# Performance work log

Measured on AMD Instinct MI355X. Metric: run time of the kernel, lower is better.

The kernel has to match this reference:

```python
import jax, jax.numpy as jnp
import numpy as np

BS, T, HS, WS = 2, 4, 32, 32
HW = HS * WS
D, NH, NL, NP = 256, 8, 4, 4
HD = D // NH
DFFN = 1024


def layer_norm(x, g, b, eps=1e-5):
    mu = jnp.mean(x, axis=-1, keepdims=True)
    var = jnp.mean((x - mu) ** 2, axis=-1, keepdims=True)
    return (x - mu) * jax.lax.rsqrt(var + eps) * g + b


def bilinear_gather(val, loc, Hl, Wl):
    # val: (bs, nh, Hl*Wl, hd); loc: (bs, Lq, nh, P, 2) in [0,1], last dim (x, y)
    # matches F.grid_sample(align_corners=False, padding_mode='zeros') on grid=2*loc-1
    x = loc[..., 0] * Wl - 0.5
    y = loc[..., 1] * Hl - 0.5
    x0 = jnp.floor(x)
    y0 = jnp.floor(y)
    lx = x - x0
    ly = y - y0
    bs, Lq, nh, P = x.shape
    out = jnp.zeros((bs, nh, Lq * P, val.shape[-1]), val.dtype)
    for dy in (0, 1):
        for dx in (0, 1):
            xi = x0 + dx
            yi = y0 + dy
            w = (lx if dx else 1.0 - lx) * (ly if dy else 1.0 - ly)
            valid = (xi >= 0) & (xi < Wl) & (yi >= 0) & (yi < Hl)
            w = jnp.where(valid, w, 0.0)
            xi_c = jnp.clip(xi, 0, Wl - 1).astype(jnp.int32)
            yi_c = jnp.clip(yi, 0, Hl - 1).astype(jnp.int32)
            idx = (yi_c * Wl + xi_c).transpose(0, 2, 1, 3).reshape(bs, nh, Lq * P)
            g = jnp.take_along_axis(val, idx[..., None], axis=2)
            wt = w.transpose(0, 2, 1, 3).reshape(bs, nh, Lq * P)
            out = out + wt[..., None] * g
    return out.reshape(bs, nh, Lq, P, val.shape[-1])


def setup_inputs() -> dict:
    key = jax.random.key(0)
    ks = jax.random.split(key, 12)
    s = 0.02
    return {
        "src": jax.random.normal(ks[0], (BS, T, HW, D), jnp.float32),
        "pos": jax.random.normal(ks[1], (BS, T, HW, D), jnp.float32),
        "reference_points": jax.random.uniform(ks[2], (BS, T * HW, NL, 2), jnp.float32),
        "value_proj_w": jax.random.normal(ks[3], (D, D), jnp.float32) * s,
        "value_proj_b": jnp.zeros((D,), jnp.float32),
        "sampling_offsets_w": jax.random.normal(ks[4], (D, NH * NL * NP * 2), jnp.float32) * s,
        "sampling_offsets_b": jax.random.normal(ks[5], (NH * NL * NP * 2,), jnp.float32) * s,
        "attn_weights_w": jax.random.normal(ks[6], (D, NH * NL * NP), jnp.float32) * s,
        "attn_weights_b": jnp.zeros((NH * NL * NP,), jnp.float32),
        "output_proj_w": jax.random.normal(ks[7], (D, D), jnp.float32) * s,
        "output_proj_b": jnp.zeros((D,), jnp.float32),
        "norm1_g": jnp.ones((D,), jnp.float32),
        "norm1_b": jnp.zeros((D,), jnp.float32),
        "linear1_w": jax.random.normal(ks[8], (D, DFFN), jnp.float32) * s,
        "linear1_b": jnp.zeros((DFFN,), jnp.float32),
        "linear2_w": jax.random.normal(ks[9], (DFFN, D), jnp.float32) * s,
        "linear2_b": jnp.zeros((D,), jnp.float32),
        "norm2_g": jnp.ones((D,), jnp.float32),
        "norm2_b": jnp.zeros((D,), jnp.float32),
        "spatial_shapes": np.array([[HS, WS]] * NL, np.int32),
        "level_start_index": np.arange(NL, dtype=np.int32) * HW,
    }


def reference(src, pos, reference_points, value_proj_w, value_proj_b,
              sampling_offsets_w, sampling_offsets_b, attn_weights_w, attn_weights_b,
              output_proj_w, output_proj_b, norm1_g, norm1_b,
              linear1_w, linear1_b, linear2_w, linear2_b, norm2_g, norm2_b,
              spatial_shapes, level_start_index):
    bs, t, hw, d = src.shape
    Lq = t * hw
    x = src.reshape(bs, Lq, d)
    q = x  # module never adds pos in forward (with_pos_embed unused)
    value = (x @ value_proj_w + value_proj_b).reshape(bs, Lq, NH, HD)
    offsets = (q @ sampling_offsets_w + sampling_offsets_b).reshape(bs, Lq, NH, NL, NP, 2)
    aw = jax.nn.softmax((q @ attn_weights_w + attn_weights_b).reshape(bs, Lq, NH, NL * NP), axis=-1)
    aw = aw.reshape(bs, Lq, NH, NL, NP)
    ss = np.asarray(spatial_shapes)
    lsi = np.asarray(level_start_index)
    offset_normalizer = jnp.asarray(ss[:, ::-1].copy(), src.dtype)  # (L, 2) = (W, H)
    sampling_locations = reference_points[:, :, None, :, None, :] + offsets / offset_normalizer[None, None, None, :, None, :]
    attn_out = jnp.zeros((bs, NH, Lq, HD), src.dtype)
    for l in range(NL):
        Hl, Wl = int(ss[l, 0]), int(ss[l, 1])
        start = int(lsi[l])
        v_l = value[:, start:start + Hl * Wl].transpose(0, 2, 1, 3)  # (bs, nh, HlWl, hd)
        samp = bilinear_gather(v_l, sampling_locations[:, :, :, l], Hl, Wl)  # (bs, nh, Lq, P, hd)
        w_l = aw[:, :, :, l].transpose(0, 2, 1, 3)  # (bs, nh, Lq, P)
        attn_out = attn_out + jnp.sum(samp * w_l[..., None], axis=3)
    attn_out = attn_out.transpose(0, 2, 1, 3).reshape(bs, Lq, d) @ output_proj_w + output_proj_b
    x = layer_norm(x + attn_out, norm1_g, norm1_b)
    ffn = jax.nn.relu(x @ linear1_w + linear1_b) @ linear2_w + linear2_b
    x = layer_norm(x + ffn, norm2_g, norm2_b)
    return x.reshape(bs, t, hw, d), sampling_locations
```

## Files before the change

### kernel.cpp

```cpp
#include <hip/hip_runtime.h>
#include <math.h>

#define ROWS   8192
#define LQ     4096
#define NHEAD  8
#define NLVL   4
#define NPTS   4
#define HDIM   32

typedef __attribute__((ext_vector_type(8))) short v8s;
typedef __attribute__((ext_vector_type(4))) float v4f;

__device__ __forceinline__ unsigned short f2bf(float x) {
    unsigned int u = __float_as_uint(x);
    u += 0x7fffu + ((u >> 16) & 1u);
    return (unsigned short)(u >> 16);
}
__device__ __forceinline__ float bf2f(unsigned short x) {
    return __uint_as_float(((unsigned int)x) << 16);
}

__device__ __forceinline__ void glds16(const void* g, void* l) {
    __builtin_amdgcn_global_load_lds(
        (const __attribute__((address_space(1))) unsigned int*)g,
        (__attribute__((address_space(3))) unsigned int*)l, 16, 0, 0);
}

__device__ __forceinline__ void trans_tile(const float* __restrict__ in,
                                           unsigned short* __restrict__ out,
                                           int K, int N, int ldout, int n_off,
                                           int bx, int by, int tid)
{
    __shared__ float t[32][33];
    int tx = tid & 31, ty = tid >> 5;
    int k0 = by << 5, n0 = bx << 5;
    #pragma unroll
    for (int i = 0; i < 4; i++)
        t[ty + i * 8][tx] = in[(size_t)(k0 + ty + i * 8) * N + n0 + tx];
    __syncthreads();
    #pragma unroll
    for (int i = 0; i < 4; i++)
        out[(size_t)(n_off + n0 + ty + i * 8) * ldout + k0 + tx] = f2bf(t[tx][ty + i * 8]);
}

__global__ __launch_bounds__(256) void prep_k(
    const float* __restrict__ src, unsigned short* __restrict__ src_bf,
    const float* __restrict__ vw, const float* __restrict__ ofw,
    const float* __restrict__ aww, const float* __restrict__ pw,
    const float* __restrict__ w1, const float* __restrict__ w2,
    unsigned short* __restrict__ Btcat, unsigned short* __restrict__ pwT,
    unsigned short* __restrict__ w1T, unsigned short* __restrict__ w2T,
    const float* __restrict__ vb, const float* __restrict__ ofb,
    const float* __restrict__ awb, float* __restrict__ biascat)
{
    int bid = blockIdx.x, tid = threadIdx.x;
    if (bid < 2048) {
        int i = bid * 256 + tid;
        float4 v = ((const float4*)src)[i];
        ushort4 o;
        o.x = f2bf(v.x); o.y = f2bf(v.y); o.z = f2bf(v.z); o.w = f2bf(v.w);
        ((ushort4*)src_bf)[i] = o;
    } else if (bid < 2112) {
        int t = bid - 2048; trans_tile(vw, Btcat, 256, 256, 256, 0, t & 7, t >> 3, tid);
    } else if (bid < 2176) {
        int t = bid - 2112; trans_tile(ofw, Btcat, 256, 256, 256, 256, t & 7, t >> 3, tid);
    } else if (bid < 2208) {
        int t = bid - 2176; trans_tile(aww, Btcat, 256, 128, 256, 512, t & 3, t >> 2, tid);
    } else if (bid < 2272) {
        int t = bid - 2208; trans_tile(pw, pwT, 256, 256, 256, 0, t & 7, t >> 3, tid);
    } else if (bid < 2528) {
        int t = bid - 2272; trans_tile(w1, w1T, 256, 1024, 256, 0, t & 31, t >> 5, tid);
    } else if (bid < 2784) {
        int t = bid - 2528; trans_tile(w2, w2T, 1024, 256, 1024, 0, t & 7, t >> 3, tid);
    } else {
        biascat[tid] = vb[tid];
        biascat[tid + 256] = ofb[tid];
        if (tid < 128) biascat[tid + 512] = awb[tid];
    }
}

template<bool PROJ, bool OUTBF, bool RELU, bool RES>
__global__ __launch_bounds__(256) void mfma_gemm_k(
    const unsigned short* __restrict__ A,
    const unsigned short* __restrict__ Bt,
    const float* __restrict__ bias,
    const float* __restrict__ res,
    void* __restrict__ Cout,
    unsigned short* __restrict__ vbf,
    int M, int N, int K)
{
    __shared__ __align__(16) unsigned short As[4096];
    __shared__ __align__(16) unsigned short Bs[2048];
    const int tid = threadIdx.x;
    const int row0 = blockIdx.y << 7, col0 = blockIdx.x << 6;
    const int wid = tid >> 6, lane = tid & 63;
    const int wm = wid & 1, wn = wid >> 1;
    const int lr = lane & 15, kq = lane >> 4;

    v4f acc[4][2];
    #pragma unroll
    for (int i = 0; i < 4; i++)
        #pragma unroll
        for (int j = 0; j < 2; j++) acc[i][j] = (v4f){0.f, 0.f, 0.f, 0.f};

    for (int k0 = 0; k0 < K; k0 += 32) {
        __syncthreads();
        #pragma unroll
        for (int i = 0; i < 2; i++) {
            int c = wid * 128 + i * 64 + lane;
            int row = c >> 2;
            int kk = ((c & 3) + (row >> 2)) & 3;
            glds16(A + (size_t)(row0 + row) * K + k0 + kk * 8,
                   &As[(wid * 128 + i * 64) * 8]);
        }
        {
            int c = wid * 64 + lane;
            int row = c >> 2;
            int kk = ((c & 3) + (row >> 2)) & 3;
            glds16(Bt + (size_t)(col0 + row) * K + k0 + kk * 8,
                   &Bs[wid * 512]);
        }
        __syncthreads();
        v8s bf[2];
        #pragma unroll
        for (int nt = 0; nt < 2; nt++) {
            int row = wn * 32 + nt * 16 + lr;
            int s = (kq - (row >> 2)) & 3;
            bf[nt] = *(const v8s*)(&Bs[(row * 4 + s) * 8]);
        }
        #pragma unroll
        for (int mt = 0; mt < 4; mt++) {
            int row = wm * 64 + mt * 16 + lr;
            int s = (kq - (row >> 2)) & 3;
            v8s af = *(const v8s*)(&As[(row * 4 + s) * 8]);
            #pragma unroll
            for (int nt = 0; nt < 2; nt++)
                acc[mt][nt] = __builtin_amdgcn_mfma_f32_16x16x32_bf16(af, bf[nt], acc[mt][nt], 0, 0, 0);
        }
    }

    const int rq = lane >> 4;
    #pragma unroll
    for (int mt = 0; mt < 4; mt++) {
        #pragma unroll
        for (int nt = 0; nt < 2; nt++) {
            int col = col0 + wn * 32 + nt * 16 + lr;
            float bv = bias[col];
            #pragma unroll
            for (int i = 0; i < 4; i++) {
                int row = row0 + wm * 64 + mt * 16 + rq * 4 + i;
                float v = acc[mt][nt][i] + bv;
                if (RELU) v = fmaxf(v, 0.f);
                if (RES)  v += res[(size_t)row * N + col];
                if (PROJ) {
                    if (col0 < 256) {
                        int b = row >> 12, rb = row & 4095;
                        int l = rb >> 10, pix = rb & 1023;
                        int h = col >> 5, d = col & 31;
                        size_t idx = ((size_t)(((b << 2) + l) * 8 + h) << 15) + (pix << 5) + d;
                        vbf[idx] = f2bf(v);
                    } else {
                        ((float*)Cout)[(size_t)row * 384 + col - 256] = v;
                    }
                } else if (OUTBF) {
                    ((unsigned short*)Cout)[(size_t)row * N + col] = f2bf(v);
                } else {
                    ((float*)Cout)[(size_t)row * N + col] = v;
                }
            }
        }
    }
}

__global__ __launch_bounds__(256) void fused_gather_k(
    const float* __restrict__ po,
    const unsigned short* __restrict__ vbf,
    const float* __restrict__ refp,
    float* __restrict__ out_loc,
    unsigned short* __restrict__ attn_bf)
{
    int tid = threadIdx.x;
    int u = tid >> 5, l = (tid >> 3) & 3, d4 = tid & 7;
    int gid = blockIdx.x * 8 + u;
    int h = gid & 7, r = gid >> 3;
    int b = r >> 12;
    const float* prow = po + (size_t)r * 384;

    float2 rp = *(const float2*)(refp + (size_t)r * 8 + l * 2);

    float off[8];
    *(float4*)(off)     = *(const float4*)(prow + h * 32 + l * 8);
    *(float4*)(off + 4) = *(const float4*)(prow + h * 32 + l * 8 + 4);
    float locv[8];
    #pragma unroll
    for (int k = 0; k < 8; k++)
        locv[k] = ((k & 1) ? rp.y : rp.x) + off[k] * (1.f / 32.f);
    out_loc[(size_t)r * 256 + h * 32 + l * 8 + d4] = locv[d4];

    float w4[4];
    *(float4*)(w4) = *(const float4*)(prow + 256 + h * 16 + l * 4);
    float m = fmaxf(fmaxf(w4[0], w4[1]), fmaxf(w4[2], w4[3]));
    m = fmaxf(m, __shfl_xor(m, 8));
    m = fmaxf(m, __shfl_xor(m, 16));
    float s = 0.f;
    #pragma unroll
    for (int p = 0; p < 4; p++) { w4[p] = __expf(w4[p] - m); s += w4[p]; }
    s += __shfl_xor(s, 8);
    s += __shfl_xor(s, 16);
    float inv = 1.f / s;

    const unsigned short* vbase =
        vbf + (((size_t)(((b << 2) + l) * 8 + h)) << 15) + d4 * 4;
    ushort4 uv[16];
    float cw[16];
    #pragma unroll
    for (int p = 0; p < 4; p++) {
        float xf = locv[p * 2] * 32.f - 0.5f, yf = locv[p * 2 + 1] * 32.f - 0.5f;
        float x0f = floorf(xf), y0f = floorf(yf);
        float fx = xf - x0f, fy = yf - y0f;
        int x0 = (int)x0f, y0 = (int)y0f;
        float wgt = w4[p] * inv;
        #pragma unroll
        for (int dy = 0; dy < 2; dy++) {
            #pragma unroll
            for (int dx = 0; dx < 2; dx++) {
                int idx = p * 4 + dy * 2 + dx;
                int xi = x0 + dx, yi = y0 + dy;
                float wt = (dx ? fx : 1.f - fx) * (dy ? fy : 1.f - fy);
                bool valid = (xi >= 0) & (xi < 32) & (yi >= 0) & (yi < 32);
                int xc = min(max(xi, 0), 31), yc = min(max(yi, 0), 31);
                cw[idx] = valid ? (wgt * wt) : 0.f;
                uv[idx] = *(const ushort4*)(vbase + (size_t)((yc << 5) + xc) * 32);
            }
        }
    }
    float4 acc = {0.f, 0.f, 0.f, 0.f};
    #pragma unroll
    for (int idx = 0; idx < 16; idx++) {
        float c = cw[idx];
        acc.x += c * bf2f(uv[idx].x); acc.y += c * bf2f(uv[idx].y);
        acc.z += c * bf2f(uv[idx].z); acc.w += c * bf2f(uv[idx].w);
    }
    acc.x += __shfl_xor(acc.x, 8);  acc.y += __shfl_xor(acc.y, 8);
    acc.z += __shfl_xor(acc.z, 8);  acc.w += __shfl_xor(acc.w, 8);
    acc.x += __shfl_xor(acc.x, 16); acc.y += __shfl_xor(acc.y, 16);
    acc.z += __shfl_xor(acc.z, 16); acc.w += __shfl_xor(acc.w, 16);
    if (l == 0) {
        ushort4 o;
        o.x = f2bf(acc.x); o.y = f2bf(acc.y); o.z = f2bf(acc.z); o.w = f2bf(acc.w);
        *(ushort4*)(attn_bf + (size_t)r * 256 + h * 32 + d4 * 4) = o;
    }
}

template<bool WRITE_BF>
__global__ __launch_bounds__(256) void layernorm_k(
    float* __restrict__ x, const float* __restrict__ g, const float* __restrict__ b,
    unsigned short* __restrict__ xbf)
{
    int lane = threadIdx.x & 63;
    int wv = threadIdx.x >> 6;
    int row = blockIdx.x * 4 + wv;
    int c = lane << 2;
    float4 v = *(const float4*)(x + (size_t)row * 256 + c);
    float s = v.x + v.y + v.z + v.w;
    #pragma unroll
    for (int o = 1; o < 64; o <<= 1) s += __shfl_xor(s, o);
    float mu = s * (1.f / 256.f);
    float d0 = v.x - mu, d1 = v.y - mu, d2 = v.z - mu, d3 = v.w - mu;
    float vs = d0 * d0 + d1 * d1 + d2 * d2 + d3 * d3;
    #pragma unroll
    for (int o = 1; o < 64; o <<= 1) vs += __shfl_xor(vs, o);
    float rstd = rsqrtf(vs * (1.f / 256.f) + 1e-5f);
    float4 gg = *(const float4*)(g + c);
    float4 bb = *(const float4*)(b + c);
    float4 o4;
    o4.x = d0 * rstd * gg.x + bb.x;
    o4.y = d1 * rstd * gg.y + bb.y;
    o4.z = d2 * rstd * gg.z + bb.z;
    o4.w = d3 * rstd * gg.w + bb.w;
    *(float4*)(x + (size_t)row * 256 + c) = o4;
    if (WRITE_BF) {
        ushort4 ob;
        ob.x = f2bf(o4.x); ob.y = f2bf(o4.y); ob.z = f2bf(o4.z); ob.w = f2bf(o4.w);
        *(ushort4*)(xbf + (size_t)row * 256 + c) = ob;
    }
}

extern "C" void kernel_launch(void* const* d_in, const int* in_sizes, int n_in,
                              void* d_out, int out_size, void* d_ws, size_t ws_size,
                              hipStream_t stream)
{
    const float* src   = (const float*)d_in[0];
    const float* refp  = (const float*)d_in[2];
    const float* vw    = (const float*)d_in[3];
    const float* vb    = (const float*)d_in[4];
    const float* ofw   = (const float*)d_in[5];
    const float* ofb   = (const float*)d_in[6];
    const float* aww   = (const float*)d_in[7];
    const float* awb   = (const float*)d_in[8];
    const float* pw    = (const float*)d_in[9];
    const float* pb    = (const float*)d_in[10];
    const float* g1    = (const float*)d_in[11];
    const float* b1    = (const float*)d_in[12];
    const float* w1    = (const float*)d_in[13];
    const float* bi1   = (const float*)d_in[14];
    const float* w2    = (const float*)d_in[15];
    const float* bi2   = (const float*)d_in[16];
    const float* g2    = (const float*)d_in[17];
    const float* b2    = (const float*)d_in[18];

    float* ws = (float*)d_ws;
    float*          po        = ws;
    float*          x1        = ws + 3145728;
    unsigned short* value_bf  = (unsigned short*)(ws + 5242880);
    unsigned short* src_bf    = (unsigned short*)(ws + 6291456);
    unsigned short* x1_bf     = (unsigned short*)(ws + 7340032);
    unsigned short* attn_bf   = (unsigned short*)(ws + 8388608);
    unsigned short* hidden_bf = (unsigned short*)(ws + 9437184);
    unsigned short* Btcat     = (unsigned short*)(ws + 13631488);
    unsigned short* pwT       = (unsigned short*)(ws + 13713408);
    unsigned short* w1T       = (unsigned short*)(ws + 13746176);
    unsigned short* w2T       = (unsigned short*)(ws + 13877248);
    float*          biascat   = ws + 14008320;

    float* out_x   = (float*)d_out;
    float* out_loc = out_x + 2097152;

    dim3 blk(256);

    prep_k<<<2785, blk, 0, stream>>>(src, src_bf, vw, ofw, aww, pw, w1, w2,
                                     Btcat, pwT, w1T, w2T, vb, ofb, awb, biascat);

    mfma_gemm_k<true, false, false, false><<<dim3(10, 64), blk, 0, stream>>>(
        src_bf, Btcat, biascat, nullptr, po, value_bf, ROWS, 640, 256);

    fused_gather_k<<<8192, blk, 0, stream>>>(po, value_bf, refp, out_loc, attn_bf);

    mfma_gemm_k<false, false, false, true><<<dim3(4, 64), blk, 0, stream>>>(
        attn_bf, pwT, pb, src, x1, nullptr, ROWS, 256, 256);
    layernorm_k<true><<<2048, blk, 0, stream>>>(x1, g1, b1, x1_bf);

    mfma_gemm_k<false, true, true, false><<<dim3(16, 64), blk, 0, stream>>>(
        x1_bf, w1T, bi1, nullptr, hidden_bf, nullptr, ROWS, 1024, 256);
    mfma_gemm_k<false, false, false, true><<<dim3(4, 64), blk, 0, stream>>>(
        hidden_bf, w2T, bi2, x1, out_x, nullptr, ROWS, 256, 1024);
    layernorm_k<false><<<2048, blk, 0, stream>>>(out_x, g2, b2, nullptr);
}
```

Measured before the change: 191.1 us.

## Remap deformable gather to one wave per query-head with 16-byte loads

The gather kernel is remapped so each 64-lane wave handles one (query, head) pair. Each lane owns one (level, point) sample and an 8-element chunk of the head dimension, instead of a 32-thread group where each thread looped over 4 points with 4-element loads. This shrinks per-thread register arrays (16 loaded vectors down to 4), uses 16-byte value loads, and doubles the grid so more threads hide gather latency. The cost is more cross-lane shuffles, since the softmax and accumulation reductions now span the whole wave, and twice as many blocks.

Measured after the change: 198.1 us. +3.7%, slower.

```diff
diff --git a/kernel.cpp b/kernel.cpp
--- a/kernel.cpp
+++ b/kernel.cpp
@@ -10,6 +10,7 @@
 
 typedef __attribute__((ext_vector_type(8))) short v8s;
 typedef __attribute__((ext_vector_type(4))) float v4f;
+typedef __attribute__((ext_vector_type(8))) unsigned short v8u;
 
 __device__ __forceinline__ unsigned short f2bf(float x) {
     unsigned int u = __float_as_uint(x);
@@ -180,75 +181,79 @@
     unsigned short* __restrict__ attn_bf)
 {
     int tid = threadIdx.x;
-    int u = tid >> 5, l = (tid >> 3) & 3, d4 = tid & 7;
-    int gid = blockIdx.x * 8 + u;
+    int wv = tid >> 6, lane = tid & 63;
+    int lp = lane >> 2, dq = lane & 3;
+    int l = lp >> 2;
+    int gid = blockIdx.x * 4 + wv;
     int h = gid & 7, r = gid >> 3;
     int b = r >> 12;
     const float* prow = po + (size_t)r * 384;
 
     float2 rp = *(const float2*)(refp + (size_t)r * 8 + l * 2);
-
-    float off[8];
-    *(float4*)(off)     = *(const float4*)(prow + h * 32 + l * 8);
-    *(float4*)(off + 4) = *(const float4*)(prow + h * 32 + l * 8 + 4);
-    float locv[8];
-    #pragma unroll
-    for (int k = 0; k < 8; k++)
-        locv[k] = ((k & 1) ? rp.y : rp.x) + off[k] * (1.f / 32.f);
-    out_loc[(size_t)r * 256 + h * 32 + l * 8 + d4] = locv[d4];
-
-    float w4[4];
-    *(float4*)(w4) = *(const float4*)(prow + 256 + h * 16 + l * 4);
-    float m = fmaxf(fmaxf(w4[0], w4[1]), fmaxf(w4[2], w4[3]));
+    float2 off = *(const float2*)(prow + h * 32 + lp * 2);
+    float lx = rp.x + off.x * (1.f / 32.f);
+    float ly = rp.y + off.y * (1.f / 32.f);
+    if (dq == 0)
+        *(float2*)(out_loc + (size_t)r * 256 + h * 32 + lp * 2) = make_float2(lx, ly);
+
+    float wl = prow[256 + h * 16 + lp];
+    float m = wl;
+    m = fmaxf(m, __shfl_xor(m, 4));
     m = fmaxf(m, __shfl_xor(m, 8));
     m = fmaxf(m, __shfl_xor(m, 16));
-    float s = 0.f;
-    #pragma unroll
-    for (int p = 0; p < 4; p++) { w4[p] = __expf(w4[p] - m); s += w4[p]; }
+    m = fmaxf(m, __shfl_xor(m, 32));
+    float e = __expf(wl - m);
+    float s = e;
+    s += __shfl_xor(s, 4);
     s += __shfl_xor(s, 8);
     s += __shfl_xor(s, 16);
-    float inv = 1.f / s;
-
+    s += __shfl_xor(s, 32);
+    float wgt = e / s;
+
+    float xf = lx * 32.f - 0.5f, yf = ly * 32.f - 0.5f;
+    float x0f = floorf(xf), y0f = floorf(yf);
+    float fx = xf - x0f, fy = yf - y0f;
+    int x0 = (int)x0f, y0 = (int)y0f;
     const unsigned short* vbase =
-        vbf + (((size_t)(((b << 2) + l) * 8 + h)) << 15) + d4 * 4;
-    ushort4 uv[16];
-    float cw[16];
-    #pragma unroll
-    for (int p = 0; p < 4; p++) {
-        float xf = locv[p * 2] * 32.f - 0.5f, yf = locv[p * 2 + 1] * 32.f - 0.5f;
-        float x0f = floorf(xf), y0f = floorf(yf);
-        float fx = xf - x0f, fy = yf - y0f;
-        int x0 = (int)x0f, y0 = (int)y0f;
-        float wgt = w4[p] * inv;
-        #pragma unroll
-        for (int dy = 0; dy < 2; dy++) {
-            #pragma unroll
-            for (int dx = 0; dx < 2; dx++) {
-                int idx = p * 4 + dy * 2 + dx;
-                int xi = x0 + dx, yi = y0 + dy;
-                float wt = (dx ? fx : 1.f - fx) * (dy ? fy : 1.f - fy);
-                bool valid = (xi >= 0) & (xi < 32) & (yi >= 0) & (yi < 32);
-                int xc = min(max(xi, 0), 31), yc = min(max(yi, 0), 31);
-                cw[idx] = valid ? (wgt * wt) : 0.f;
-                uv[idx] = *(const ushort4*)(vbase + (size_t)((yc << 5) + xc) * 32);
-            }
-        }
-    }
-    float4 acc = {0.f, 0.f, 0.f, 0.f};
-    #pragma unroll
-    for (int idx = 0; idx < 16; idx++) {
+        vbf + (((size_t)(((b << 2) + l) * 8 + h)) << 15) + dq * 8;
+
+    v8u uv[4];
+    float cw[4];
+    #pragma unroll
+    for (int dy = 0; dy < 2; dy++) {
+        #pragma unroll
+        for (int dx = 0; dx < 2; dx++) {
+            int idx = dy * 2 + dx;
+            int xi = x0 + dx, yi = y0 + dy;
+            float wt = (dx ? fx : 1.f - fx) * (dy ? fy : 1.f - fy);
+            bool valid = (xi >= 0) & (xi < 32) & (yi >= 0) & (yi < 32);
+            int xc = min(max(xi, 0), 31), yc = min(max(yi, 0), 31);
+            cw[idx] = valid ? (wgt * wt) : 0.f;
+            uv[idx] = *(const v8u*)(vbase + (size_t)((yc << 5) + xc) * 32);
+        }
+    }
+    float acc[8];
+    #pragma unroll
+    for (int k = 0; k < 8; k++) acc[k] = 0.f;
+    #pragma unroll
+    for (int idx = 0; idx < 4; idx++) {
         float c = cw[idx];
-        acc.x += c * bf2f(uv[idx].x); acc.y += c * bf2f(uv[idx].y);
-        acc.z += c * bf2f(uv[idx].z); acc.w += c * bf2f(uv[idx].w);
-    }
-    acc.x += __shfl_xor(acc.x, 8);  acc.y += __shfl_xor(acc.y, 8);
-    acc.z += __shfl_xor(acc.z, 8);  acc.w += __shfl_xor(acc.w, 8);
-    acc.x += __shfl_xor(acc.x, 16); acc.y += __shfl_xor(acc.y, 16);
-    acc.z += __shfl_xor(acc.z, 16); acc.w += __shfl_xor(acc.w, 16);
-    if (l == 0) {
-        ushort4 o;
-        o.x = f2bf(acc.x); o.y = f2bf(acc.y); o.z = f2bf(acc.z); o.w = f2bf(acc.w);
-        *(ushort4*)(attn_bf + (size_t)r * 256 + h * 32 + d4 * 4) = o;
+        #pragma unroll
+        for (int k = 0; k < 8; k++)
+            acc[k] += c * bf2f(uv[idx][k]);
+    }
+    #pragma unroll
+    for (int k = 0; k < 8; k++) {
+        acc[k] += __shfl_xor(acc[k], 4);
+        acc[k] += __shfl_xor(acc[k], 8);
+        acc[k] += __shfl_xor(acc[k], 16);
+        acc[k] += __shfl_xor(acc[k], 32);
+    }
+    if (lane < 4) {
+        v8u o;
+        #pragma unroll
+        for (int k = 0; k < 8; k++) o[k] = f2bf(acc[k]);
+        *(v8u*)(attn_bf + (size_t)r * 256 + h * 32 + lane * 8) = o;
     }
 }
 
@@ -334,7 +339,7 @@
     mfma_gemm_k<true, false, false, false><<<dim3(10, 64), blk, 0, stream>>>(
         src_bf, Btcat, biascat, nullptr, po, value_bf, ROWS, 640, 256);
 
-    fused_gather_k<<<8192, blk, 0, stream>>>(po, value_bf, refp, out_loc, attn_bf);
+    fused_gather_k<<<16384, blk, 0, stream>>>(po, value_bf, refp, out_loc, attn_bf);
 
     mfma_gemm_k<false, false, false, true><<<dim3(4, 64), blk, 0, stream>>>(
         attn_bf, pwT, pb, src, x1, nullptr, ROWS, 256, 256);
```
